# Kernel tuning notes

Hardware: AMD Instinct MI355X
Metric: run time of the kernel (lower is better)

The kernel has to match this reference:

```python
import jax, jax.numpy as jnp
import numpy as np

C = 64
SHIFT = 3
NEIGHBOR_SIZES = (3, 5, 7)  # dilation = 1 for all levels
NUM_GROUPS = 8


def conv2d(x, w, b, padding=0, groups=1):
    out = jax.lax.conv_general_dilated(
        x, w, (1, 1), [(padding, padding), (padding, padding)],
        dimension_numbers=('NCHW', 'OIHW', 'NCHW'),
        feature_group_count=groups)
    return out + b[None, :, None, None]


def natten_level(q, k, v, rpb, ks):
    # q,k,v: (B,H,W,C) channels-last; rpb: (2ks-1, 2ks-1); dilation=1.
    # NATTEN semantics: window of size ks x ks centered at each query, clamped
    # (shifted) at image borders so it always lies fully inside the image.
    B, H, W, Cc = q.shape
    r = ks // 2
    i = jnp.arange(H); ni = jnp.clip(i - r, 0, H - ks)   # window row starts
    j = jnp.arange(W); nj = jnp.clip(j - r, 0, W - ks)   # window col starts
    ar = jnp.arange(ks)
    ii = ni[:, None] + ar[None, :]                        # (H,ks) neighbor rows
    jj = nj[:, None] + ar[None, :]                        # (W,ks) neighbor cols
    kn = k[:, ii][:, :, :, jj]                            # (B,H,ks,W,ks,C)
    attn = jnp.einsum('bhwc,bhpwqc->bhwpq', q, kn)        # (B,H,W,ks,ks)
    # relative-position-bias lookup: row start pi = (ks-1) + ni - i
    pi = (ks - 1) + ni - i                                # (H,)
    pj = (ks - 1) + nj - j                                # (W,)
    bias = rpb[(pi[:, None] + ar[None, :])[:, None, :, None],
               (pj[:, None] + ar[None, :])[None, :, None, :]]  # (H,W,ks,ks)
    attn = attn + bias[None]
    attn = jax.nn.softmax(attn.reshape(B, H, W, ks * ks), axis=-1)
    attn = attn.reshape(B, H, W, ks, ks)
    vn = v[:, ii][:, :, :, jj]                            # (B,H,ks,W,ks,C)
    return jnp.einsum('bhwpq,bhpwqc->bhwc', attn, vn)


def _forward(sup_frame, key_frame, conv_smooth_w, conv_smooth_b,
             conv_reduce_w, conv_reduce_b, v_w0, v_b0, v_w1, v_b1,
             v_w2, v_b2, rpb0, rpb1, rpb2, fusion_w, fusion_b):
    p = SHIFT
    outs = [sup_frame]  # original (pre-shift) support features
    # shift-roll spatial correlation
    shifts = [(sh, sw) for sh in (-p, 0, p) for sw in (-p, 0, p)
              if not (sh == 0 and sw == 0)]
    padded = jnp.pad(sup_frame, ((0, 0), (0, 0), (p, p), (p, p)))
    parts = jnp.split(padded, NUM_GROUPS, axis=1)
    shifted = jnp.concatenate(
        [jnp.roll(parts[g], shifts[g], axis=(2, 3)) for g in range(NUM_GROUPS)],
        axis=1)[..., p:-p, p:-p]
    shifted = conv2d(shifted, conv_smooth_w, conv_smooth_b, padding=1,
                     groups=NUM_GROUPS)
    sup2 = conv2d(jnp.concatenate([sup_frame, shifted], axis=1),
                  conv_reduce_w, conv_reduce_b)
    # multi-scale neighborhood attention (single head)
    q = jnp.transpose(key_frame, (0, 2, 3, 1))
    k = jnp.transpose(sup2, (0, 2, 3, 1))
    v_ws = (v_w0, v_w1, v_w2); v_bs = (v_b0, v_b1, v_b2)
    rpbs = (rpb0, rpb1, rpb2)
    for lvl, ks in enumerate(NEIGHBOR_SIZES):
        v = jnp.transpose(conv2d(sup2, v_ws[lvl], v_bs[lvl]), (0, 2, 3, 1))
        agg = natten_level(q, k, v, rpbs[lvl], ks)
        outs.append(jnp.transpose(agg, (0, 3, 1, 2)))
    fused = jnp.concatenate(outs, axis=1)  # (B, 4*C, H, W)
    return jax.nn.relu(conv2d(fused, fusion_w, fusion_b, padding=1))


def setup_inputs() -> dict:
    key = jax.random.key(0)
    ks = jax.random.split(key, 20)
    B, H, W = 4, 96, 96
    s = 0.05
    d = {}
    d['sup_frame'] = jax.random.normal(ks[0], (B, C, H, W), jnp.float32)
    d['key_frame'] = jax.random.normal(ks[1], (B, C, H, W), jnp.float32)
    d['conv_smooth_w'] = jax.random.normal(ks[2], (C, C // NUM_GROUPS, 3, 3), jnp.float32) * s
    d['conv_smooth_b'] = jnp.zeros((C,), jnp.float32)
    d['conv_reduce_w'] = jax.random.normal(ks[3], (C, 2 * C, 1, 1), jnp.float32) * s
    d['conv_reduce_b'] = jnp.zeros((C,), jnp.float32)
    for i, nk in enumerate(NEIGHBOR_SIZES):
        d[f'v_w{i}'] = jax.random.normal(ks[4 + i], (C, C, 1, 1), jnp.float32) * s
        d[f'v_b{i}'] = jnp.zeros((C,), jnp.float32)
        d[f'rpb{i}'] = jax.random.normal(ks[8 + i], (2 * nk - 1, 2 * nk - 1), jnp.float32) * 0.02
    d['fusion_w'] = jax.random.normal(ks[12], (C, C * (len(NEIGHBOR_SIZES) + 1), 3, 3), jnp.float32) * s
    d['fusion_b'] = jnp.zeros((C,), jnp.float32)
    return d


def reference(sup_frame, key_frame, conv_smooth_w, conv_smooth_b,
              conv_reduce_w, conv_reduce_b, v_w0, v_b0, v_w1, v_b1,
              v_w2, v_b2, rpb0, rpb1, rpb2, fusion_w, fusion_b):
    return _forward(sup_frame, key_frame, conv_smooth_w, conv_smooth_b,
                    conv_reduce_w, conv_reduce_b, v_w0, v_b0, v_w1, v_b1,
                    v_w2, v_b2, rpb0, rpb1, rpb2, fusion_w, fusion_b)
```

## Files before the change

kernel.cpp:

```cpp
#include <hip/hip_runtime.h>
#include <hip/hip_bf16.h>

#define HW 9216
#define NPX 36864

typedef __attribute__((ext_vector_type(8))) short short8;
typedef __attribute__((ext_vector_type(4))) float f32x4;

static __device__ __forceinline__ unsigned short f2bf(float x) {
    union { __hip_bfloat16 h; unsigned short u; } c; c.h = __float2bfloat16(x); return c.u;
}
static __device__ __forceinline__ float bfl(unsigned int u){ return __uint_as_float(u << 16); }
static __device__ __forceinline__ float bfh(unsigned int u){ return __uint_as_float(u & 0xffff0000u); }

__global__ __launch_bounds__(256) void prep_weights(
    const float* __restrict__ rw, const float* __restrict__ vw0,
    const float* __restrict__ vw1, const float* __restrict__ vw2,
    const float* __restrict__ fw,
    float* __restrict__ rwT, unsigned short* __restrict__ vwF, unsigned short* __restrict__ fwF)
{
    int idx = blockIdx.x * 256 + threadIdx.x;
    if (idx < 8192) {
        int c = idx & 63, i = idx >> 6;
        rwT[idx] = rw[c * 128 + i];
    } else if (idx < 20480) {
        int e = idx - 8192;
        int j = e & 7, lane = (e >> 3) & 63, kf = (e >> 9) & 1, nt = (e >> 10) & 3, lvl = e >> 12;
        int co = nt * 16 + (lane & 15);
        int k = kf * 32 + (lane >> 4) * 8 + j;
        const float* vw = (lvl == 0) ? vw0 : ((lvl == 1) ? vw1 : vw2);
        vwF[e] = f2bf(vw[co * 64 + k]);
    } else if (idx < 167936) {
        int e = idx - 20480;
        int j = e & 7, lane = (e >> 3) & 63, nt = (e >> 9) & 3, kc = e >> 11;
        int co = nt * 16 + (lane & 15);
        int k = kc * 32 + ((lane >> 4) << 3) + j;
        int tap = k >> 8, ci = k & 255;
        fwF[e] = f2bf(fw[co * 2304 + ci * 9 + tap]);
    }
}

__global__ void pack_kernel(const float* __restrict__ key, const float* __restrict__ sup,
                            __hip_bfloat16* __restrict__ qB, __hip_bfloat16* __restrict__ fused)
{
    __shared__ float lk[32][33], ls[32][33];
    int tx = threadIdx.x, ty = threadIdx.y;
    int x0 = blockIdx.x * 32, c0 = blockIdx.y * 32;
    int z = blockIdx.z; int b = z / 96, y = z - b * 96;
    #pragma unroll
    for (int i = 0; i < 32; i += 8) {
        int c = c0 + ty + i;
        lk[ty + i][tx] = key[((b * 64 + c) * 96 + y) * 96 + x0 + tx];
        ls[ty + i][tx] = sup[((b * 64 + c) * 96 + y) * 96 + x0 + tx];
    }
    __syncthreads();
    #pragma unroll
    for (int i = 0; i < 32; i += 8) {
        int px = (b * 96 + y) * 96 + x0 + ty + i;
        qB[px * 64 + c0 + tx]     = __hip_bfloat16(lk[tx][ty + i]);
        fused[px * 256 + c0 + tx] = __hip_bfloat16(ls[tx][ty + i]);
    }
}

__global__ __launch_bounds__(256) void shift_smooth(const float* __restrict__ sup,
    const float* __restrict__ w, const float* __restrict__ bias, float* __restrict__ smooth)
{
    __shared__ __align__(16) float tile[8][34][36];
    int bid = blockIdx.x;
    int half = bid & 1;
    int sj   = (bid >> 1) % 9;
    int grp  = (bid / 18) & 7;
    int b    = bid / 144;
    int sby = sj / 3, sbx = sj % 3;
    int Y0 = sby * 32, X0 = sbx * 32;
    int sh = 3 * ((grp >= 5) - (grp < 3));
    int mm = (grp < 3) ? grp : ((grp < 5) ? ((grp == 3) ? 0 : 2) : (grp - 5));
    int sw = 3 * mm - 3;
    int t = threadIdx.x;

    const float* supg = sup + (size_t)(b * 64 + grp * 8) * HW;
    #pragma unroll
    for (int pp = 0; pp < 5; pp++) {
        int pos = pp * 256 + t;
        if (pos < 1156) {
            int r = pos / 34, u = pos - r * 34;
            int yy = Y0 - 1 + r, xx = X0 - 1 + u;
            int ys = yy - sh, xs = xx - sw;
            bool ok = (yy >= 0) & (yy < 96) & (xx >= 0) & (xx < 96) &
                      (ys >= 0) & (ys < 96) & (xs >= 0) & (xs < 96);
            int addr = ok ? (ys * 96 + xs) : 0;
            #pragma unroll
            for (int ic = 0; ic < 8; ic++) {
                float v = supg[(size_t)ic * HW + addr];
                tile[ic][r][u] = ok ? v : 0.f;
            }
        }
    }
    __syncthreads();

    int c = __builtin_amdgcn_readfirstlane(grp * 8 + half * 4 + (t >> 6));
    int lane = t & 63;
    int ty4 = lane >> 3, tx4 = lane & 7;
    int py0 = ty4 * 4, x0r = tx4 * 4;

    float bz = bias[c];
    float acc[4][4];
    #pragma unroll
    for (int jr = 0; jr < 4; jr++)
        #pragma unroll
        for (int j = 0; j < 4; j++) acc[jr][j] = bz;

    const float* wp = w + c * 72;
    for (int ic = 0; ic < 8; ic++) {
        float wr[9];
        #pragma unroll
        for (int q = 0; q < 9; q++) wr[q] = wp[ic * 9 + q];
        #pragma unroll
        for (int rr = 0; rr < 6; rr++) {
            float4 fa = *(const float4*)&tile[ic][py0 + rr][x0r];
            float4 fb4 = *(const float4*)&tile[ic][py0 + rr][x0r + 4];
            float f[6] = {fa.x, fa.y, fa.z, fa.w, fb4.x, fb4.y};
            #pragma unroll
            for (int ky = 0; ky < 3; ky++) {
                int jr = rr - ky;
                if (jr >= 0 && jr < 4) {
                    #pragma unroll
                    for (int j = 0; j < 4; j++)
                        acc[jr][j] += wr[ky*3]*f[j] + wr[ky*3+1]*f[j+1] + wr[ky*3+2]*f[j+2];
                }
            }
        }
    }

    float* op = smooth + ((size_t)(b * 64 + c) * 96 + Y0 + py0) * 96 + X0 + x0r;
    #pragma unroll
    for (int jr = 0; jr < 4; jr++) {
        float4 st = {acc[jr][0], acc[jr][1], acc[jr][2], acc[jr][3]};
        *(float4*)(op + (size_t)jr * 96) = st;
    }
}

__global__ __launch_bounds__(256) void reduce_kernel(const float* __restrict__ sup,
    const float* __restrict__ smooth, const float* __restrict__ rwT,
    const float* __restrict__ rb, float* __restrict__ sup2)
{
    __shared__ __align__(16) float wlds[8192];
    int t = threadIdx.x;
    #pragma unroll
    for (int e = 0; e < 8; e++) {
        int idx = (e * 256 + t) * 4;
        *(float4*)&wlds[idx] = *(const float4*)&rwT[idx];
    }
    __syncthreads();

    int lane = t & 63, wq = t >> 6;
    int px = blockIdx.x * 64 + lane;
    int b = px / HW; int rem = px - b * HW;
    const float* s1 = sup + (size_t)b * 64 * HW + rem;
    const float* s2 = smooth + (size_t)b * 64 * HW + rem;
    float acc[16];
    #pragma unroll
    for (int j = 0; j < 16; j++) acc[j] = rb[wq * 16 + j];

    #pragma unroll 8
    for (int i = 0; i < 64; i++) {
        float v = s1[i * HW];
        const float* wr = &wlds[i * 64 + wq * 16];
        float4 w0 = *(const float4*)wr, w1 = *(const float4*)(wr + 4);
        float4 w2 = *(const float4*)(wr + 8), w3 = *(const float4*)(wr + 12);
        acc[0] += w0.x * v;  acc[1] += w0.y * v;  acc[2] += w0.z * v;  acc[3] += w0.w * v;
        acc[4] += w1.x * v;  acc[5] += w1.y * v;  acc[6] += w1.z * v;  acc[7] += w1.w * v;
        acc[8] += w2.x * v;  acc[9] += w2.y * v;  acc[10] += w2.z * v; acc[11] += w2.w * v;
        acc[12] += w3.x * v; acc[13] += w3.y * v; acc[14] += w3.z * v; acc[15] += w3.w * v;
    }
    #pragma unroll 8
    for (int i = 0; i < 64; i++) {
        float v = s2[i * HW];
        const float* wr = &wlds[(64 + i) * 64 + wq * 16];
        float4 w0 = *(const float4*)wr, w1 = *(const float4*)(wr + 4);
        float4 w2 = *(const float4*)(wr + 8), w3 = *(const float4*)(wr + 12);
        acc[0] += w0.x * v;  acc[1] += w0.y * v;  acc[2] += w0.z * v;  acc[3] += w0.w * v;
        acc[4] += w1.x * v;  acc[5] += w1.y * v;  acc[6] += w1.z * v;  acc[7] += w1.w * v;
        acc[8] += w2.x * v;  acc[9] += w2.y * v;  acc[10] += w2.z * v; acc[11] += w2.w * v;
        acc[12] += w3.x * v; acc[13] += w3.y * v; acc[14] += w3.z * v; acc[15] += w3.w * v;
    }

    float* op = sup2 + (size_t)px * 64 + wq * 16;
    #pragma unroll
    for (int j = 0; j < 16; j += 4) { float4 st = {acc[j], acc[j+1], acc[j+2], acc[j+3]}; *(float4*)(op + j) = st; }
}

template<int KS>
__device__ __forceinline__ void level_softmax(int qc, int y, int x, int ty0, int tx0,
        const _Float16* rpbl, const _Float16* dots_row, _Float16* out_row, bool inplace)
{
    constexpr int R = KS / 2, KK = KS * KS, NB = 2 * KS - 1;
    constexpr int NE = (KK + 7) / 8;
    int ni = min(max(y - R, 0), 96 - KS), nj = min(max(x - R, 0), 96 - KS);
    int lyL = ni - (ty0 - 3), lxL = nj - (tx0 - 3);
    int br = KS - 1 + ni - y, bc = KS - 1 + nj - x;
    float sv[NE];
    float mx = -1e30f;
    #pragma unroll
    for (int i = 0; i < NE; i++) {
        int e = qc + i * 8;
        if (e < KK) {
            int ey = e / KS, ex = e - ey * KS;
            float s = (float)dots_row[(lyL + ey) * 14 + lxL + ex] + (float)rpbl[(br + ey) * NB + bc + ex];
            sv[i] = s; mx = fmaxf(mx, s);
        } else sv[i] = -1e30f;
    }
    mx = fmaxf(mx, __shfl_xor(mx, 8)); mx = fmaxf(mx, __shfl_xor(mx, 16)); mx = fmaxf(mx, __shfl_xor(mx, 32));
    float sum = 0.f;
    #pragma unroll
    for (int i = 0; i < NE; i++) { sv[i] = __expf(sv[i] - mx); sum += sv[i]; }
    sum += __shfl_xor(sum, 8); sum += __shfl_xor(sum, 16); sum += __shfl_xor(sum, 32);
    float inv = 1.f / sum;
    #pragma unroll
    for (int i = 0; i < NE; i++) {
        int e = qc + i * 8;
        if (e < KK) {
            int ey = e / KS, ex = e - ey * KS;
            _Float16 wv16 = (_Float16)(sv[i] * inv);
            if (inplace) ((_Float16*)dots_row)[(lyL + ey) * 14 + lxL + ex] = wv16;
            else out_row[e] = wv16;
        }
    }
}

__global__ __launch_bounds__(256) void natten_fused(
    const __hip_bfloat16* __restrict__ qB, const float* __restrict__ sup2,
    const unsigned short* __restrict__ vwF,
    const float* __restrict__ vb0, const float* __restrict__ vb1, const float* __restrict__ vb2,
    const float* __restrict__ rpb0, const float* __restrict__ rpb1, const float* __restrict__ rpb2,
    __hip_bfloat16* __restrict__ fused)
{
    __shared__ __align__(16) unsigned short khalo[140 * 72];
    __shared__ __align__(16) unsigned short qlds[32 * 72];
    __shared__ _Float16 dotsF[32][148];
    __shared__ _Float16 a3[32][12];
    __shared__ _Float16 a5[32][28];
    __shared__ _Float16 rlds[276];

    int t = threadIdx.x;
    int bb = blockIdx.y;
    int tx0 = (blockIdx.x % 12) * 8, ty0 = (blockIdx.x / 12) * 4;
    const float* kb = sup2 + (size_t)bb * HW * 64;

    for (int e = t; e < 275; e += 256) {
        float v = (e < 169) ? rpb2[e] : ((e < 250) ? rpb1[e - 169] : rpb0[e - 250]);
        rlds[e] = (_Float16)v;
    }

    for (int it = 0; it < 9; it++) {
        int qidx = it * 256 + t;
        if (qidx < 2240) {
            int cq = qidx & 15, pos = qidx >> 4;
            int py = pos / 14, pxx = pos - py * 14;
            int gy = min(max(ty0 - 3 + py, 0), 95);
            int gx = min(max(tx0 - 3 + pxx, 0), 95);
            float4 v = *(const float4*)(kb + (((size_t)gy * 96 + gx) << 6) + cq * 4);
            ushort4 pk = {f2bf(v.x), f2bf(v.y), f2bf(v.z), f2bf(v.w)};
            *(ushort4*)&khalo[pos * 72 + cq * 4] = pk;
        }
    }
    if (t < 256) {
        int px = t >> 3, seg = t & 7;
        short8 v = *(const short8*)((const unsigned short*)qB +
            ((size_t)(bb * HW + (ty0 + (px >> 3)) * 96 + tx0 + (px & 7)) << 6) + seg * 8);
        *(short8*)&qlds[px * 72 + seg * 8] = v;
    }
    __syncthreads();

    int lane = t & 63, wv = t >> 6;
    int lm = lane & 15, quad = lane >> 4;

    #pragma unroll
    for (int ni = 0; ni < 3; ni++) {
        int nt = wv + ni * 4;
        if (nt <= 8) {
            int hp = nt * 16 + lm;
            int hpr = min(hp, 139);
            f32x4 acc0 = {0.f, 0.f, 0.f, 0.f}, acc1 = {0.f, 0.f, 0.f, 0.f};
            #pragma unroll
            for (int kt = 0; kt < 2; kt++) {
                short8 bfrag = *(const short8*)&khalo[hpr * 72 + kt * 32 + quad * 8];
                short8 a0 = *(const short8*)&qlds[lm * 72 + kt * 32 + quad * 8];
                short8 a1 = *(const short8*)&qlds[(16 + lm) * 72 + kt * 32 + quad * 8];
                acc0 = __builtin_amdgcn_mfma_f32_16x16x32_bf16(a0, bfrag, acc0, 0, 0, 0);
                acc1 = __builtin_amdgcn_mfma_f32_16x16x32_bf16(a1, bfrag, acc1, 0, 0, 0);
            }
            if (hp < 140) {
                #pragma unroll
                for (int r = 0; r < 4; r++) {
                    dotsF[quad * 4 + r][hp]      = (_Float16)acc0[r];
                    dotsF[16 + quad * 4 + r][hp] = (_Float16)acc1[r];
                }
            }
        }
    }
    __syncthreads();

    int pxl = wv * 8 + (lane & 7);
    int qc = lane >> 3;
    int pty = pxl >> 3, ptx = pxl & 7;
    int y = ty0 + pty, x = tx0 + ptx;

    int ni7 = min(max(y - 3, 0), 89), nj7 = min(max(x - 3, 0), 89);
    int ly = ni7 - (ty0 - 3), lx = nj7 - (tx0 - 3);

    level_softmax<3>(qc, y, x, ty0, tx0, rlds + 250, &dotsF[pxl][0], &a3[pxl][0], false);
    level_softmax<5>(qc, y, x, ty0, tx0, rlds + 169, &dotsF[pxl][0], &a5[pxl][0], false);
    level_softmax<7>(qc, y, x, ty0, tx0, rlds,       &dotsF[pxl][0], nullptr,     true);

    int ni5 = min(max(y - 2, 0), 91), nj5 = min(max(x - 2, 0), 91);
    int ni3 = min(max(y - 1, 0), 93), nj3 = min(max(x - 1, 0), 93);
    int di5 = ni5 - ni7, dj5 = nj5 - nj7, di3 = ni3 - ni7, dj3 = nj3 - nj7;

    float s2[3][8];
    #pragma unroll
    for (int l = 0; l < 3; l++)
        #pragma unroll
        for (int j = 0; j < 8; j++) s2[l][j] = 0.f;

    #pragma unroll 1
    for (int oy = 0; oy < 7; oy++) {
        #pragma unroll
        for (int ox = 0; ox < 7; ox++) {
            const unsigned short* kp = &khalo[((ly + oy) * 14 + lx + ox) * 72 + qc * 8];
            uint4 ka = *(const uint4*)kp;
            float kv[8] = {bfl(ka.x), bfh(ka.x), bfl(ka.y), bfh(ka.y),
                           bfl(ka.z), bfh(ka.z), bfl(ka.w), bfh(ka.w)};
            float w7 = (float)dotsF[pxl][(ly + oy) * 14 + lx + ox];
            #pragma unroll
            for (int j = 0; j < 8; j++) s2[2][j] += w7 * kv[j];
            int e5y = oy - di5, e5x = ox - dj5;
            if ((unsigned)e5y < 5u && (unsigned)e5x < 5u) {
                float w5 = (float)a5[pxl][e5y * 5 + e5x];
                #pragma unroll
                for (int j = 0; j < 8; j++) s2[1][j] += w5 * kv[j];
            }
            int e3y = oy - di3, e3x = ox - dj3;
            if ((unsigned)e3y < 3u && (unsigned)e3x < 3u) {
                float w3 = (float)a3[pxl][e3y * 3 + e3x];
                #pragma unroll
                for (int j = 0; j < 8; j++) s2[0][j] += w3 * kv[j];
            }
        }
    }
    __syncthreads();

    unsigned short* sproj = khalo;
    #pragma unroll
    for (int l = 0; l < 3; l++) {
        unsigned int pk[4];
        #pragma unroll
        for (int j = 0; j < 4; j++)
            pk[j] = (unsigned int)f2bf(s2[l][2*j]) | ((unsigned int)f2bf(s2[l][2*j+1]) << 16);
        uint4 sv = {pk[0], pk[1], pk[2], pk[3]};
        *(uint4*)&sproj[(l * 32 + pxl) * 72 + qc * 8] = sv;
    }
    __syncthreads();

    if (wv < 3) {
        int l = wv;
        const float* vbl = (l == 0) ? vb0 : ((l == 1) ? vb1 : vb2);
        #pragma unroll
        for (int mt = 0; mt < 2; mt++) {
            f32x4 acc[4];
            #pragma unroll
            for (int nt = 0; nt < 4; nt++) acc[nt] = (f32x4){0.f, 0.f, 0.f, 0.f};
            #pragma unroll
            for (int kf = 0; kf < 2; kf++) {
                short8 a = *(const short8*)&sproj[(l * 32 + mt * 16 + lm) * 72 + kf * 32 + quad * 8];
                #pragma unroll
                for (int nt = 0; nt < 4; nt++) {
                    short8 bfr = *(const short8*)&vwF[(((l * 4 + nt) * 2 + kf) * 64 + lane) * 8];
                    acc[nt] = __builtin_amdgcn_mfma_f32_16x16x32_bf16(a, bfr, acc[nt], 0, 0, 0);
                }
            }
            #pragma unroll
            for (int nt = 0; nt < 4; nt++)
                #pragma unroll
                for (int r = 0; r < 4; r++) {
                    int p = mt * 16 + quad * 4 + r;
                    int co = nt * 16 + lm;
                    int py = p >> 3, pxx = p & 7;
                    size_t off = ((size_t)(bb * HW + (ty0 + py) * 96 + tx0 + pxx) << 8) + (l + 1) * 64 + co;
                    fused[off] = __hip_bfloat16(acc[nt][r] + vbl[co]);
                }
        }
    }
}

__global__ __launch_bounds__(256) void fusion_mfma(
    const __hip_bfloat16* __restrict__ fB, const unsigned short* __restrict__ fwF,
    const float* __restrict__ fb, float* __restrict__ out)
{
    __shared__ __align__(16) unsigned char smem[33408];
    unsigned short* ah = (unsigned short*)smem;
    float* lds_out = (float*)smem;
    int t = threadIdx.x;
    int wv = t >> 6, lane = t & 63, lm = lane & 15, quad = lane >> 4;
    int X0 = blockIdx.x * 16, Y0 = blockIdx.y * 8, b = blockIdx.z;
    const unsigned short* fBu = (const unsigned short*)fB;

    f32x4 acc[2][4] = {};

    for (int chunk = 0; chunk < 4; chunk++) {
        __syncthreads();
        #pragma unroll
        for (int ee = 0; ee < 6; ee++) {
            int e = ee * 256 + t;
            if (e < 1440) {
                int seg = e & 7, hp = e >> 3;
                int hy = hp / 18, hx = hp - hy * 18;
                int gy = Y0 - 1 + hy, gx = X0 - 1 + hx;
                bool ok = (gy >= 0) & (gy < 96) & (gx >= 0) & (gx < 96);
                short8 v = {};
                if (ok) v = *(const short8*)(fBu + (((size_t)(b * HW + gy * 96 + gx)) << 8) + chunk * 64 + seg * 8);
                *(short8*)&ah[hp * 72 + seg * 8] = v;
            }
        }
        __syncthreads();
        #pragma unroll
        for (int ky = 0; ky < 3; ky++) {
            #pragma unroll
            for (int kx = 0; kx < 3; kx++) {
                #pragma unroll
                for (int kf = 0; kf < 2; kf++) {
                    int kc = (ky * 3 + kx) * 8 + chunk * 2 + kf;
                    const unsigned short* bp = fwF + ((size_t)(kc * 4) * 64 + lane) * 8;
                    short8 b0 = *(const short8*)(bp);
                    short8 b1 = *(const short8*)(bp + 512);
                    short8 b2 = *(const short8*)(bp + 1024);
                    short8 b3 = *(const short8*)(bp + 1536);
                    #pragma unroll
                    for (int mt = 0; mt < 2; mt++) {
                        int R = 2 * wv + mt;
                        short8 a = *(const short8*)&ah[((R + ky) * 18 + lm + kx) * 72 + kf * 32 + quad * 8];
                        acc[mt][0] = __builtin_amdgcn_mfma_f32_16x16x32_bf16(a, b0, acc[mt][0], 0, 0, 0);
                        acc[mt][1] = __builtin_amdgcn_mfma_f32_16x16x32_bf16(a, b1, acc[mt][1], 0, 0, 0);
                        acc[mt][2] = __builtin_amdgcn_mfma_f32_16x16x32_bf16(a, b2, acc[mt][2], 0, 0, 0);
                        acc[mt][3] = __builtin_amdgcn_mfma_f32_16x16x32_bf16(a, b3, acc[mt][3], 0, 0, 0);
                    }
                }
            }
        }
    }

    __syncthreads();
    #pragma unroll
    for (int mt = 0; mt < 2; mt++)
        #pragma unroll
        for (int nt = 0; nt < 4; nt++)
            #pragma unroll
            for (int r = 0; r < 4; r++) {
                int p = (2 * wv + mt) * 16 + quad * 4 + r;
                int co = nt * 16 + lm;
                lds_out[co * 130 + p] = acc[mt][nt][r];
            }
    __syncthreads();

    int p2 = t & 127, py = p2 >> 4, px2 = p2 & 15;
    float* ob = out + ((size_t)(b * 64) * 96 + Y0 + py) * 96 + X0 + px2;
    #pragma unroll 4
    for (int i = 0; i < 32; i++) {
        int co = (t >> 7) * 32 + i;
        float v = lds_out[co * 130 + p2] + fb[co];
        ob[(size_t)co * HW] = v > 0.f ? v : 0.f;
    }
}

extern "C" void kernel_launch(void* const* d_in, const int* in_sizes, int n_in,
                              void* d_out, int out_size, void* d_ws, size_t ws_size,
                              hipStream_t stream) {
    const float* sup = (const float*)d_in[0];
    const float* key = (const float*)d_in[1];
    const float* smw = (const float*)d_in[2];
    const float* smb = (const float*)d_in[3];
    const float* rw  = (const float*)d_in[4];
    const float* rb  = (const float*)d_in[5];
    const float *vw[3], *vb[3], *rpb[3];
    if (in_sizes[8] == 25) {
        for (int l = 0; l < 3; l++) {
            vw[l]  = (const float*)d_in[6 + 3 * l];
            vb[l]  = (const float*)d_in[7 + 3 * l];
            rpb[l] = (const float*)d_in[8 + 3 * l];
        }
    } else {
        for (int l = 0; l < 3; l++) {
            vw[l]  = (const float*)d_in[6 + 2 * l];
            vb[l]  = (const float*)d_in[7 + 2 * l];
            rpb[l] = (const float*)d_in[12 + l];
        }
    }
    const float* fw = (const float*)d_in[15];
    const float* fb = (const float*)d_in[16];
    float* out = (float*)d_out;

    float* wsf    = (float*)d_ws;
    float* smooth = wsf;
    float* sup2   = wsf + 2359296;
    __hip_bfloat16* qBuf = (__hip_bfloat16*)(wsf + 4718592);
    float* rwT    = wsf + 7077888;
    unsigned short* vwF = (unsigned short*)(wsf + 7086080);
    __hip_bfloat16* fusedB = (__hip_bfloat16*)(wsf + 7092224);
    unsigned short* fwF    = (unsigned short*)(wsf + 11810816);

    prep_weights<<<dim3(656), dim3(256), 0, stream>>>(rw, vw[0], vw[1], vw[2], fw, rwT, vwF, fwF);
    pack_kernel<<<dim3(3, 2, 384), dim3(32, 8), 0, stream>>>(key, sup, qBuf, fusedB);
    shift_smooth<<<dim3(576), dim3(256), 0, stream>>>(sup, smw, smb, smooth);
    reduce_kernel<<<dim3(576), dim3(256), 0, stream>>>(sup, smooth, rwT, rb, sup2);
    natten_fused<<<dim3(288, 4), dim3(256), 0, stream>>>(qBuf, sup2, vwF,
        vb[0], vb[1], vb[2], rpb[0], rpb[1], rpb[2], fusedB);
    fusion_mfma<<<dim3(6, 12, 4), dim3(256), 0, stream>>>(fusedB, fwF, fb, out);
}
```

Baseline: 203.0 us.

## Run the 1x1 reduce conv on bf16 MFMA and store sup2 as bf16

New measurement: 188.4 us. -7.2%, faster.

```diff
diff --git a/kernel.cpp b/kernel.cpp
--- a/kernel.cpp
+++ b/kernel.cpp
@@ -17,12 +17,15 @@
     const float* __restrict__ rw, const float* __restrict__ vw0,
     const float* __restrict__ vw1, const float* __restrict__ vw2,
     const float* __restrict__ fw,
-    float* __restrict__ rwT, unsigned short* __restrict__ vwF, unsigned short* __restrict__ fwF)
+    unsigned short* __restrict__ rwF, unsigned short* __restrict__ vwF, unsigned short* __restrict__ fwF)
 {
     int idx = blockIdx.x * 256 + threadIdx.x;
     if (idx < 8192) {
-        int c = idx & 63, i = idx >> 6;
-        rwT[idx] = rw[c * 128 + i];
+        int e = idx;
+        int j = e & 7, lane = (e >> 3) & 63, kf = (e >> 9) & 3, nt = e >> 11;
+        int co = nt * 16 + (lane & 15);
+        int k = kf * 32 + (lane >> 4) * 8 + j;
+        rwF[e] = f2bf(rw[co * 128 + k]);
     } else if (idx < 20480) {
         int e = idx - 8192;
         int j = e & 7, lane = (e >> 3) & 63, kf = (e >> 9) & 1, nt = (e >> 10) & 3, lvl = e >> 12;
@@ -140,54 +143,53 @@
     }
 }
 
-__global__ __launch_bounds__(256) void reduce_kernel(const float* __restrict__ sup,
-    const float* __restrict__ smooth, const float* __restrict__ rwT,
-    const float* __restrict__ rb, float* __restrict__ sup2)
-{
-    __shared__ __align__(16) float wlds[8192];
+__global__ __launch_bounds__(256) void reduce_mfma(
+    const __hip_bfloat16* __restrict__ fB, const float* __restrict__ smooth,
+    const unsigned short* __restrict__ rwF, const float* __restrict__ rb,
+    unsigned short* __restrict__ sup2B)
+{
+    __shared__ __align__(16) unsigned short A[64 * 136];
     int t = threadIdx.x;
-    #pragma unroll
-    for (int e = 0; e < 8; e++) {
-        int idx = (e * 256 + t) * 4;
-        *(float4*)&wlds[idx] = *(const float4*)&rwT[idx];
-    }
-    __syncthreads();
-
-    int lane = t & 63, wq = t >> 6;
-    int px = blockIdx.x * 64 + lane;
-    int b = px / HW; int rem = px - b * HW;
-    const float* s1 = sup + (size_t)b * 64 * HW + rem;
-    const float* s2 = smooth + (size_t)b * 64 * HW + rem;
-    float acc[16];
-    #pragma unroll
-    for (int j = 0; j < 16; j++) acc[j] = rb[wq * 16 + j];
-
-    #pragma unroll 8
-    for (int i = 0; i < 64; i++) {
-        float v = s1[i * HW];
-        const float* wr = &wlds[i * 64 + wq * 16];
-        float4 w0 = *(const float4*)wr, w1 = *(const float4*)(wr + 4);
-        float4 w2 = *(const float4*)(wr + 8), w3 = *(const float4*)(wr + 12);
-        acc[0] += w0.x * v;  acc[1] += w0.y * v;  acc[2] += w0.z * v;  acc[3] += w0.w * v;
-        acc[4] += w1.x * v;  acc[5] += w1.y * v;  acc[6] += w1.z * v;  acc[7] += w1.w * v;
-        acc[8] += w2.x * v;  acc[9] += w2.y * v;  acc[10] += w2.z * v; acc[11] += w2.w * v;
-        acc[12] += w3.x * v; acc[13] += w3.y * v; acc[14] += w3.z * v; acc[15] += w3.w * v;
-    }
-    #pragma unroll 8
-    for (int i = 0; i < 64; i++) {
-        float v = s2[i * HW];
-        const float* wr = &wlds[(64 + i) * 64 + wq * 16];
-        float4 w0 = *(const float4*)wr, w1 = *(const float4*)(wr + 4);
-        float4 w2 = *(const float4*)(wr + 8), w3 = *(const float4*)(wr + 12);
-        acc[0] += w0.x * v;  acc[1] += w0.y * v;  acc[2] += w0.z * v;  acc[3] += w0.w * v;
-        acc[4] += w1.x * v;  acc[5] += w1.y * v;  acc[6] += w1.z * v;  acc[7] += w1.w * v;
-        acc[8] += w2.x * v;  acc[9] += w2.y * v;  acc[10] += w2.z * v; acc[11] += w2.w * v;
-        acc[12] += w3.x * v; acc[13] += w3.y * v; acc[14] += w3.z * v; acc[15] += w3.w * v;
-    }
-
-    float* op = sup2 + (size_t)px * 64 + wq * 16;
-    #pragma unroll
-    for (int j = 0; j < 16; j += 4) { float4 st = {acc[j], acc[j+1], acc[j+2], acc[j+3]}; *(float4*)(op + j) = st; }
+    int gpx0 = blockIdx.x * 64;
+    int b = gpx0 / HW, rem0 = gpx0 - b * HW;
+    const unsigned short* fBu = (const unsigned short*)fB;
+
+    #pragma unroll
+    for (int it = 0; it < 2; it++) {
+        int e = it * 256 + t;
+        int px = e >> 3, seg = e & 7;
+        short8 v = *(const short8*)(fBu + ((size_t)(gpx0 + px) << 8) + seg * 8);
+        *(short8*)&A[px * 136 + seg * 8] = v;
+    }
+    #pragma unroll
+    for (int it = 0; it < 16; it++) {
+        int e = it * 256 + t;
+        int px = e & 63, ci = e >> 6;
+        float v = smooth[(size_t)(b * 64 + ci) * HW + rem0 + px];
+        A[px * 136 + 64 + ci] = f2bf(v);
+    }
+    __syncthreads();
+
+    int lane = t & 63, wv = t >> 6;
+    int lm = lane & 15, quad = lane >> 4;
+    f32x4 acc[4] = {};
+    #pragma unroll
+    for (int kf = 0; kf < 4; kf++) {
+        short8 a = *(const short8*)&A[(wv * 16 + lm) * 136 + kf * 32 + quad * 8];
+        #pragma unroll
+        for (int nt = 0; nt < 4; nt++) {
+            short8 bfr = *(const short8*)&rwF[((nt * 4 + kf) * 64 + lane) * 8];
+            acc[nt] = __builtin_amdgcn_mfma_f32_16x16x32_bf16(a, bfr, acc[nt], 0, 0, 0);
+        }
+    }
+    #pragma unroll
+    for (int nt = 0; nt < 4; nt++)
+        #pragma unroll
+        for (int r = 0; r < 4; r++) {
+            int px = wv * 16 + quad * 4 + r;
+            int co = nt * 16 + lm;
+            sup2B[(size_t)(gpx0 + px) * 64 + co] = f2bf(acc[nt][r] + rb[co]);
+        }
 }
 
 template<int KS>
@@ -229,7 +231,7 @@
 }
 
 __global__ __launch_bounds__(256) void natten_fused(
-    const __hip_bfloat16* __restrict__ qB, const float* __restrict__ sup2,
+    const __hip_bfloat16* __restrict__ qB, const unsigned short* __restrict__ sup2B,
     const unsigned short* __restrict__ vwF,
     const float* __restrict__ vb0, const float* __restrict__ vb1, const float* __restrict__ vb2,
     const float* __restrict__ rpb0, const float* __restrict__ rpb1, const float* __restrict__ rpb2,
@@ -245,23 +247,23 @@
     int t = threadIdx.x;
     int bb = blockIdx.y;
     int tx0 = (blockIdx.x % 12) * 8, ty0 = (blockIdx.x / 12) * 4;
-    const float* kb = sup2 + (size_t)bb * HW * 64;
+    const unsigned short* kbB = sup2B + (size_t)bb * HW * 64;
 
     for (int e = t; e < 275; e += 256) {
         float v = (e < 169) ? rpb2[e] : ((e < 250) ? rpb1[e - 169] : rpb0[e - 250]);
         rlds[e] = (_Float16)v;
     }
 
-    for (int it = 0; it < 9; it++) {
-        int qidx = it * 256 + t;
-        if (qidx < 2240) {
-            int cq = qidx & 15, pos = qidx >> 4;
+    #pragma unroll
+    for (int it = 0; it < 5; it++) {
+        int e = it * 256 + t;
+        if (e < 1120) {
+            int seg = e & 7, pos = e >> 3;
             int py = pos / 14, pxx = pos - py * 14;
             int gy = min(max(ty0 - 3 + py, 0), 95);
             int gx = min(max(tx0 - 3 + pxx, 0), 95);
-            float4 v = *(const float4*)(kb + (((size_t)gy * 96 + gx) << 6) + cq * 4);
-            ushort4 pk = {f2bf(v.x), f2bf(v.y), f2bf(v.z), f2bf(v.w)};
-            *(ushort4*)&khalo[pos * 72 + cq * 4] = pk;
+            short8 v = *(const short8*)(kbB + (((size_t)gy * 96 + gx) << 6) + seg * 8);
+            *(short8*)&khalo[pos * 72 + seg * 8] = v;
         }
     }
     if (t < 256) {
@@ -501,18 +503,18 @@
 
     float* wsf    = (float*)d_ws;
     float* smooth = wsf;
-    float* sup2   = wsf + 2359296;
+    unsigned short* sup2B = (unsigned short*)(wsf + 2359296);
     __hip_bfloat16* qBuf = (__hip_bfloat16*)(wsf + 4718592);
-    float* rwT    = wsf + 7077888;
+    unsigned short* rwF = (unsigned short*)(wsf + 7077888);
     unsigned short* vwF = (unsigned short*)(wsf + 7086080);
     __hip_bfloat16* fusedB = (__hip_bfloat16*)(wsf + 7092224);
     unsigned short* fwF    = (unsigned short*)(wsf + 11810816);
 
-    prep_weights<<<dim3(656), dim3(256), 0, stream>>>(rw, vw[0], vw[1], vw[2], fw, rwT, vwF, fwF);
+    prep_weights<<<dim3(656), dim3(256), 0, stream>>>(rw, vw[0], vw[1], vw[2], fw, rwF, vwF, fwF);
     pack_kernel<<<dim3(3, 2, 384), dim3(32, 8), 0, stream>>>(key, sup, qBuf, fusedB);
     shift_smooth<<<dim3(576), dim3(256), 0, stream>>>(sup, smw, smb, smooth);
-    reduce_kernel<<<dim3(576), dim3(256), 0, stream>>>(sup, smooth, rwT, rb, sup2);
-    natten_fused<<<dim3(288, 4), dim3(256), 0, stream>>>(qBuf, sup2, vwF,
+    reduce_mfma<<<dim3(576), dim3(256), 0, stream>>>(fusedB, smooth, rwF, rb, sup2B);
+    natten_fused<<<dim3(288, 4), dim3(256), 0, stream>>>(qBuf, sup2B, vwF,
         vb[0], vb[1], vb[2], rpb[0], rpb[1], rpb[2], fusedB);
     fusion_mfma<<<dim3(6, 12, 4), dim3(256), 0, stream>>>(fusedB, fwF, fb, out);
 }
```
